# Kernel optimization log

Hardware: AMD Instinct MI355X
Metric: run time of the kernel (lower is better)

The kernel has to match this reference:

```python
import jax, jax.numpy as jnp
import numpy as np

N, E, D, F, L = 50000, 250000, 128, 12, 4
EPS_POS = 1e-6
EPS_LN = 1e-5


def setup_inputs() -> dict:
    key = jax.random.key(0)
    ks = iter(jax.random.split(key, 40))
    w = lambda *s: jax.random.normal(next(ks), s, dtype=jnp.float32) * 0.05
    inp = {
        'node_features': jax.random.normal(next(ks), (N, F), dtype=jnp.float32),
        'pos': jax.random.normal(next(ks), (N, 2), dtype=jnp.float32),
        'edge_attr_raw': jax.random.normal(next(ks), (E, F), dtype=jnp.float32),
        'node_proj_w': w(F, D), 'node_proj_b': jnp.zeros((D,), jnp.float32),
        'edge_proj_w': w(F, D), 'edge_proj_b': jnp.zeros((D,), jnp.float32),
        'edge_w1': w(L, 2 * D + 1, D), 'edge_b1': jnp.zeros((L, D), jnp.float32),
        'edge_w2': w(L, D, D), 'edge_b2': jnp.zeros((L, D), jnp.float32),
        'node_w1': w(L, 2 * D, D), 'node_b1': jnp.zeros((L, D), jnp.float32),
        'node_w2': w(L, D, D), 'node_b2': jnp.zeros((L, D), jnp.float32),
        'pos_w1': w(L, D + 1, 1), 'pos_b1': jnp.zeros((L, 1), jnp.float32),
        'pos_w2': w(L, 1, 1), 'pos_b2': jnp.zeros((L, 1), jnp.float32),
        'ln_g': jnp.ones((D,), jnp.float32), 'ln_b': jnp.zeros((D,), jnp.float32),
        'edge_index': jax.random.randint(next(ks), (2, E), 0, N, dtype=jnp.int32),
    }
    return inp


def reference(node_features, pos, edge_attr_raw,
              node_proj_w, node_proj_b, edge_proj_w, edge_proj_b,
              edge_w1, edge_b1, edge_w2, edge_b2,
              node_w1, node_b1, node_w2, node_b2,
              pos_w1, pos_b1, pos_w2, pos_b2,
              ln_g, ln_b, edge_index):
    src, tgt = edge_index[0], edge_index[1]
    n = node_features.shape[0]
    x = node_features @ node_proj_w + node_proj_b          # [N, D]
    # edge_projection output is concatenated then sliced away in the original
    # (edge_input[:, :2D+1]); it is mathematically dead but computed faithfully.
    _edge_attr = edge_attr_raw @ edge_proj_w + edge_proj_b  # dead
    p = pos                                                  # [N, 2]
    for l in range(L):
        xs, xt = x[src], x[tgt]                              # [E, D]
        ps, pt = p[src], p[tgt]                              # [E, 2]
        dist = jnp.linalg.norm(ps - pt, axis=1, keepdims=True)  # [E, 1]
        e_in = jnp.concatenate([xs, xt, dist], axis=1)       # [E, 2D+1]
        msg = jax.nn.silu(e_in @ edge_w1[l] + edge_b1[l]) @ edge_w2[l] + edge_b2[l]
        pos_diff = pt - ps
        pos_unit = pos_diff / (jnp.linalg.norm(pos_diff, axis=1, keepdims=True) + EPS_POS)
        pw = jax.nn.silu(jnp.concatenate([msg, dist], axis=1) @ pos_w1[l] + pos_b1[l])
        pw = pw @ pos_w2[l] + pos_b2[l]                       # [E, 1]
        p = p + jax.ops.segment_sum(pos_unit * pw, tgt, num_segments=n)
        agg = jax.ops.segment_sum(msg, tgt, num_segments=n)  # [N, D]
        n_in = jnp.concatenate([x, agg], axis=1)              # [N, 2D]
        x = x + (jax.nn.silu(n_in @ node_w1[l] + node_b1[l]) @ node_w2[l] + node_b2[l])
    mu = jnp.mean(x, axis=-1, keepdims=True)
    var = jnp.mean(jnp.square(x - mu), axis=-1, keepdims=True)
    x = (x - mu) * jax.lax.rsqrt(var + EPS_LN) * ln_g + ln_b
    return x[None]                                            # [1, N, D]
```

## Files before the change

kernel.cpp:

```cpp
#include <hip/hip_runtime.h>
#include <hip/hip_bf16.h>


#define NNODES 50000
#define NEDGES 250000
#define NTILES 3125
#define MMGRID 512
#define RGRID  1024

typedef unsigned short u16;
typedef __attribute__((ext_vector_type(8))) short bf16x8;
typedef __attribute__((ext_vector_type(4))) float floatx4;

__device__ __forceinline__ float b2f(u16 h){ unsigned u=((unsigned)h)<<16; float f; __builtin_memcpy(&f,&u,4); return f; }
__device__ __forceinline__ u16 f2b(float f){ unsigned u; __builtin_memcpy(&u,&f,4); u = u + 0x7FFFu + ((u>>16)&1u); return (u16)(u>>16); }
__device__ __forceinline__ float siluf(float x){ return x*__builtin_amdgcn_rcpf(1.f+__expf(-x)); }
__device__ __forceinline__ float ldf(const void* p, long i, int isbf){
  return isbf ? b2f(((const u16*)p)[i]) : ((const float*)p)[i];
}
__device__ __forceinline__ long swz(long row, int col){
  return (row>>4)*2048 + (long)(((col>>4)*4 + (int)(row&3))*64 + (((int)(row&15))>>2)*16 + (col&15));
}

__global__ void detect_kernel(const void* lng, int* flag){
  if (threadIdx.x==0 && blockIdx.x==0) *flag = (((const u16*)lng)[0] != 0) ? 1 : 0;
}

#define SU_W12   192
#define SU_EBW   704
#define SU_W2P   708
#define SU_PPARM 712
#define SU_PROJ  713
#define SU_CVTP  25713
#define SU_END   26104
__global__ __launch_bounds__(256) void setup_kernel(
    const void* __restrict__ ew1, const void* __restrict__ ew2,
    const void* __restrict__ nw1, const void* __restrict__ nw2,
    u16* __restrict__ packed,
    const void* __restrict__ eb2, const void* __restrict__ pw1,
    const void* __restrict__ pb1, const void* __restrict__ pw2v, const void* __restrict__ pb2,
    float* __restrict__ w2p, float* __restrict__ c2p, float* __restrict__ pparm,
    float* __restrict__ ebW,
    const void* __restrict__ nf, const void* __restrict__ npw, const void* __restrict__ npb,
    u16* __restrict__ xb,
    const void* __restrict__ pos, float* __restrict__ pf,
    const int* __restrict__ flagp)
{
  const int isbf = *flagp;
  const int b = blockIdx.x, tid = threadIdx.x;
  __shared__ float red[128];
  if (b < SU_W12){
    int t = b*256 + tid;
    int m = t >> 11; int r = t & 2047;
    int lane = r & 63; int ntk = r >> 6;
    int kk = ntk >> 3, nt = ntk & 7;
    int l = m/6, w = m%6;
    const void* src; long off;
    switch(w){
      case 0: src=ew1; off=(long)l*257*128;            break;
      case 1: src=ew1; off=(long)l*257*128 + 128*128;  break;
      case 2: src=ew2; off=(long)l*128*128;            break;
      case 3: src=nw1; off=(long)l*256*128;            break;
      case 4: src=nw1; off=(long)l*256*128 + 128*128;  break;
      default:src=nw2; off=(long)l*128*128;            break;
    }
    int c  = nt*16 + (lane & 15);
    int k0 = kk*32 + (lane >> 4)*8;
    u16 vals[8];
#pragma unroll
    for (int j=0;j<8;j++){
      long idx = off + (long)(k0+j)*128 + c;
      vals[j] = isbf ? ((const u16*)src)[idx] : f2b(((const float*)src)[idx]);
    }
    bf16x8 v; __builtin_memcpy(&v, vals, 16);
    *(bf16x8*)(packed + (long)t*8) = v;
  } else if (b < SU_EBW){
    int bb = b - SU_W12;
    int l = bb >> 7, k = bb & 127;
    if (tid < 128){
      int j = tid;
      long e2 = (long)l*16384 + (long)k*128;
      long nb = (long)l*256*128 + 128*128;
      float acc = 0.f;
      for (int d=0; d<128; d++)
        acc += ldf(ew2, e2 + d, isbf) * ldf(nw1, nb + (long)d*128 + j, isbf);
      int kk = k>>5, lane = ((k>>3)&3)*16 + (j&15), nt = j>>4, jj = k&7;
      packed[(long)(24+l)*16384 + (long)((kk*8+nt)*64 + lane)*8 + jj] = f2b(acc);
    }
  } else if (b < SU_W2P){
    int l = b - SU_EBW;
    if (tid < 128){
      int j = tid;
      long nb = (long)l*256*128 + 128*128;
      float acc = 0.f;
      for (int d=0; d<128; d++)
        acc += ldf(eb2, (long)l*128 + d, isbf) * ldf(nw1, nb + (long)d*128 + j, isbf);
      ebW[l*128+j] = acc;
    }
  } else if (b < SU_PPARM){
    int l = b - SU_W2P;
    int i = tid;
    long Woff = (long)l*128*128, poff = (long)l*129;
    if (i < 128){
      float acc = 0.f;
      for (int j=0;j<128;j++) acc += ldf(ew2, Woff + (long)i*128 + j, isbf) * ldf(pw1, poff + j, isbf);
      w2p[l*128+i] = acc;
      red[i] = ldf(eb2, (long)l*128 + i, isbf) * ldf(pw1, poff + i, isbf);
    }
    __syncthreads();
    for (int st=64; st>0; st>>=1){ if (i<st) red[i]+=red[i+st]; __syncthreads(); }
    if (i==0) c2p[l] = red[0];
  } else if (b == SU_PPARM){
    int l = tid;
    if (l < 4){
      pparm[l*4+0] = ldf(pw1, (long)l*129 + 128, isbf);
      pparm[l*4+1] = ldf(pb1, l, isbf);
      pparm[l*4+2] = ldf(pw2v, l, isbf);
      pparm[l*4+3] = ldf(pb2, l, isbf);
    }
  } else if (b < SU_CVTP){
    int n = (b - SU_PROJ)*2 + (tid>>7), d = tid & 127;
    if (n < NNODES){
      float acc = ldf(npb, d, isbf);
#pragma unroll
      for (int f=0; f<12; f++) acc += ldf(nf, (long)n*12+f, isbf) * ldf(npw, f*128+d, isbf);
      xb[swz(n, d)] = f2b(acc);
    }
  } else {
    int i = (b - SU_CVTP)*256 + tid;
    if (i < 2*NNODES) pf[i] = ldf(pos, i, isbf);
  }
}

__global__ __launch_bounds__(256) void hist_kernel(const int* __restrict__ tgt, int* __restrict__ cnt, int E){
  int i = blockIdx.x*256 + threadIdx.x;
  if (i < E) atomicAdd(&cnt[tgt[i]], 1);
}

__global__ __launch_bounds__(256) void bsum_kernel(const int* __restrict__ cnt, int* __restrict__ bsum, int N){
  int i = blockIdx.x*256 + threadIdx.x;
  int v = (i < N) ? cnt[i] : 0;
#pragma unroll
  for (int off=32; off; off>>=1) v += __shfl_down(v, off);
  __shared__ int ws[4];
  if ((threadIdx.x & 63) == 0) ws[threadIdx.x>>6] = v;
  __syncthreads();
  if (threadIdx.x == 0) bsum[blockIdx.x] = ws[0]+ws[1]+ws[2]+ws[3];
}

__global__ __launch_bounds__(256) void bscan_kernel(int* __restrict__ bsum, int nb){
  __shared__ int lds[256];
  int i = threadIdx.x;
  int v = (i < nb) ? bsum[i] : 0;
  lds[i] = v; __syncthreads();
#pragma unroll
  for (int off=1; off<256; off<<=1){
    int t = (i>=off)? lds[i-off] : 0; __syncthreads();
    lds[i] += t; __syncthreads();
  }
  if (i < nb) bsum[i] = lds[i] - v;
}

__global__ __launch_bounds__(256) void csr_kernel(
    const int* __restrict__ cnt, const int* __restrict__ bsum,
    int* __restrict__ rowptr, int* __restrict__ cursor, float* __restrict__ degf, int N)
{
  __shared__ int lds[256];
  int i = blockIdx.x*256 + threadIdx.x;
  int c = (i < N) ? cnt[i] : 0;
  lds[threadIdx.x] = c; __syncthreads();
#pragma unroll
  for (int off=1; off<256; off<<=1){
    int t = (threadIdx.x>=off)? lds[threadIdx.x-off] : 0; __syncthreads();
    lds[threadIdx.x] += t; __syncthreads();
  }
  int run = bsum[blockIdx.x] + lds[threadIdx.x] - c;
  if (i < N){
    rowptr[i] = run; cursor[i] = run; degf[i] = (float)c;
    if (i == N-1) rowptr[N] = run + c;
  }
}

__global__ __launch_bounds__(256) void scatter_kernel(
    const int* __restrict__ src, const int* __restrict__ tgt,
    int* __restrict__ cursor, int* __restrict__ permsrc, int E)
{
  int e = blockIdx.x*256 + threadIdx.x;
  if (e >= E) return;
  int t = tgt[e];
  int p = atomicAdd(&cursor[t], 1);
  permsrc[p] = src[e];
}

__global__ __launch_bounds__(256) void mm_ab_kernel(
    const u16* __restrict__ X, const u16* __restrict__ Wa, const u16* __restrict__ Wb,
    const void* __restrict__ bias, long bias_off,
    u16* __restrict__ Ab, u16* __restrict__ Bb, const int* __restrict__ flagp)
{
  extern __shared__ u16 wlds[];
  const int tid = threadIdx.x, wave = tid>>6, lane = tid&63;
  const int isbf = *flagp;
  const int lr = lane&15, lg = lane>>4;
  for (int i=tid; i<2048; i+=256){
    *(bf16x8*)(wlds + (long)i*8)          = *(const bf16x8*)(Wa + (long)i*8);
    *(bf16x8*)(wlds + 16384 + (long)i*8)  = *(const bf16x8*)(Wb + (long)i*8);
  }
  float biasv[8];
#pragma unroll
  for (int nt=0;nt<8;nt++) biasv[nt] = ldf(bias, bias_off + nt*16 + lr, isbf);
  int aoff[4];
#pragma unroll
  for (int kk=0;kk<4;kk++) aoff[kk] = ((2*kk + (lg>>1))*4 + (lr&3))*64 + (lr>>2)*16 + (lg&1)*8;
  u16* sw = wlds + 32768 + (wave<<11);
  __syncthreads();
  for (int tile = blockIdx.x*4 + wave; tile < NTILES; tile += MMGRID*4){
    const u16* xt = X + (long)tile*2048;
    bf16x8 a[4];
#pragma unroll
    for (int kk=0;kk<4;kk++) a[kk] = *(const bf16x8*)(xt + aoff[kk]);
    floatx4 accA[8], accB[8];
#pragma unroll
    for (int i=0;i<8;i++){ accA[i]=(floatx4){0,0,0,0}; accB[i]=(floatx4){0,0,0,0}; }
#pragma unroll
    for (int kk=0;kk<4;kk++){
#pragma unroll
      for (int nt=0;nt<8;nt++){
        bf16x8 ba = *(const bf16x8*)(wlds + ((kk*8+nt)*64 + lane)*8);
        accA[nt] = __builtin_amdgcn_mfma_f32_16x16x32_bf16(a[kk], ba, accA[nt], 0, 0, 0);
        bf16x8 bb = *(const bf16x8*)(wlds + 16384 + ((kk*8+nt)*64 + lane)*8);
        accB[nt] = __builtin_amdgcn_mfma_f32_16x16x32_bf16(a[kk], bb, accB[nt], 0, 0, 0);
      }
    }
    u16* at = Ab + (long)tile*2048;
#pragma unroll
    for (int r=0;r<4;r++){
#pragma unroll
      for (int nt=0;nt<8;nt++) sw[(lg*4+r)*128 + nt*16 + lr] = f2b(accA[nt][r] + biasv[nt]);
    }
#pragma unroll
    for (int j=0;j<4;j++){
      bf16x8 v = *(const bf16x8*)(sw + j*512 + lane*8);
      *(bf16x8*)(at + j*512 + lane*8) = v;
    }
    u16* bt = Bb + (long)tile*2048;
#pragma unroll
    for (int r=0;r<4;r++){
#pragma unroll
      for (int nt=0;nt<8;nt++) sw[(lg*4+r)*128 + nt*16 + lr] = f2b(accB[nt][r]);
    }
#pragma unroll
    for (int j=0;j<4;j++){
      bf16x8 v = *(const bf16x8*)(sw + j*512 + lane*8);
      *(bf16x8*)(bt + j*512 + lane*8) = v;
    }
  }
}

__global__ __launch_bounds__(256) void mm_hidden_kernel(
    const u16* __restrict__ X, const u16* __restrict__ H,
    const u16* __restrict__ W1, const u16* __restrict__ W2,
    const void* __restrict__ nb1, long nb1_off,
    const float* __restrict__ degf, const float* __restrict__ ebW,
    u16* __restrict__ hb, const int* __restrict__ flagp)
{
  extern __shared__ u16 wlds[];
  const int tid = threadIdx.x, wave = tid>>6, lane = tid&63;
  const int isbf = *flagp;
  const int lr = lane&15, lg = lane>>4;
  for (int i=tid; i<2048; i+=256){
    *(bf16x8*)(wlds + (long)i*8)          = *(const bf16x8*)(W1 + (long)i*8);
    *(bf16x8*)(wlds + 16384 + (long)i*8)  = *(const bf16x8*)(W2 + (long)i*8);
  }
  float nb1v[8], ebv[8];
#pragma unroll
  for (int nt=0;nt<8;nt++){ int col=nt*16+lr; nb1v[nt]=ldf(nb1, nb1_off+col, isbf); ebv[nt]=ebW[col]; }
  int aoff[4];
#pragma unroll
  for (int kk=0;kk<4;kk++) aoff[kk] = ((2*kk + (lg>>1))*4 + (lr&3))*64 + (lr>>2)*16 + (lg&1)*8;
  __syncthreads();
  for (int tile = blockIdx.x*4 + wave; tile < NTILES; tile += MMGRID*4){
    const u16* xt = X + (long)tile*2048;
    const u16* hr = H + ((long)tile*16 + lr)*128;
    bf16x8 ax[4], ah[4];
#pragma unroll
    for (int kk=0;kk<4;kk++){
      ax[kk] = *(const bf16x8*)(xt + aoff[kk]);
      ah[kk] = *(const bf16x8*)(hr + kk*32 + lg*8);
    }
    floatx4 acc[8];
#pragma unroll
    for (int i=0;i<8;i++) acc[i]=(floatx4){0,0,0,0};
#pragma unroll
    for (int kk=0;kk<4;kk++){
#pragma unroll
      for (int nt=0;nt<8;nt++){
        bf16x8 b1 = *(const bf16x8*)(wlds + ((kk*8+nt)*64 + lane)*8);
        acc[nt] = __builtin_amdgcn_mfma_f32_16x16x32_bf16(ax[kk], b1, acc[nt], 0, 0, 0);
        bf16x8 b2 = *(const bf16x8*)(wlds + 16384 + ((kk*8+nt)*64 + lane)*8);
        acc[nt] = __builtin_amdgcn_mfma_f32_16x16x32_bf16(ah[kk], b2, acc[nt], 0, 0, 0);
      }
    }
    float dv[4];
#pragma unroll
    for (int r=0;r<4;r++) dv[r] = degf[(long)tile*16 + lg*4 + r];
    u16* ot = hb + (long)tile*2048;
#pragma unroll
    for (int r=0;r<4;r++){
#pragma unroll
      for (int nt=0;nt<8;nt++){
        ot[(nt*4+r)*64 + lane] = f2b(siluf(acc[nt][r] + nb1v[nt] + dv[r]*ebv[nt]));
      }
    }
  }
}

template<int LN>
__global__ __launch_bounds__(256) void mm_res_kernel(
    const u16* __restrict__ H, const u16* __restrict__ W,
    const void* __restrict__ nb2, long nb2_off,
    u16* __restrict__ xb,
    const void* __restrict__ lng, const void* __restrict__ lnb, void* __restrict__ outp,
    const int* __restrict__ flagp)
{
  extern __shared__ u16 wlds[];
  const int tid = threadIdx.x, wave = tid>>6, lane = tid&63;
  const int isbf = *flagp;
  const int lr = lane&15, lg = lane>>4;
  for (int i=tid; i<2048; i+=256)
    *(bf16x8*)(wlds + (long)i*8) = *(const bf16x8*)(W + (long)i*8);
  float nb2v[8];
#pragma unroll
  for (int nt=0;nt<8;nt++) nb2v[nt] = ldf(nb2, nb2_off + nt*16 + lr, isbf);
  float gv[8], bvv[8];
  if (LN){
#pragma unroll
    for (int nt=0;nt<8;nt++){ int col=nt*16+lr; gv[nt]=ldf(lng,col,isbf); bvv[nt]=ldf(lnb,col,isbf); }
  }
  int aoff[4];
#pragma unroll
  for (int kk=0;kk<4;kk++) aoff[kk] = ((2*kk + (lg>>1))*4 + (lr&3))*64 + (lr>>2)*16 + (lg&1)*8;
  __syncthreads();
  for (int tile = blockIdx.x*4 + wave; tile < NTILES; tile += RGRID*4){
    const u16* ht = H + (long)tile*2048;
    bf16x8 a[4];
#pragma unroll
    for (int kk=0;kk<4;kk++) a[kk] = *(const bf16x8*)(ht + aoff[kk]);
    floatx4 acc[8];
#pragma unroll
    for (int i=0;i<8;i++) acc[i]=(floatx4){0,0,0,0};
#pragma unroll
    for (int kk=0;kk<4;kk++){
#pragma unroll
      for (int nt=0;nt<8;nt++){
        bf16x8 b = *(const bf16x8*)(wlds + ((kk*8+nt)*64 + lane)*8);
        acc[nt] = __builtin_amdgcn_mfma_f32_16x16x32_bf16(a[kk], b, acc[nt], 0, 0, 0);
      }
    }
    u16* xt = xb + (long)tile*2048;
#pragma unroll
    for (int r=0;r<4;r++){
#pragma unroll
      for (int nt=0;nt<8;nt++){
        int o = (nt*4+r)*64 + lane;
        float v = acc[nt][r] + nb2v[nt] + b2f(xt[o]);
        acc[nt][r] = v;
        if (!LN) xt[o] = f2b(v);
      }
    }
    if (LN){
      float s[4] = {0,0,0,0}, q[4] = {0,0,0,0};
#pragma unroll
      for (int r=0;r<4;r++){
#pragma unroll
        for (int nt=0;nt<8;nt++){ float v = acc[nt][r]; s[r] += v; q[r] += v*v; }
      }
#pragma unroll
      for (int mask=1; mask<16; mask<<=1){
#pragma unroll
        for (int r=0;r<4;r++){ s[r] += __shfl_xor(s[r], mask); q[r] += __shfl_xor(q[r], mask); }
      }
#pragma unroll
      for (int r=0;r<4;r++){
        long row = (long)tile*16 + lg*4 + r;
        float mu = s[r]*(1.f/128.f);
        float var = q[r]*(1.f/128.f) - mu*mu;
        float inv = rsqrtf(var + 1e-5f);
#pragma unroll
        for (int nt=0;nt<8;nt++){
          int col = nt*16 + lr;
          float y = (acc[nt][r]-mu)*inv*gv[nt] + bvv[nt];
          if (isbf) ((u16*)outp)[row*128+col] = f2b(y);
          else      ((float*)outp)[row*128+col] = y;
        }
      }
    }
  }
}

__global__ __launch_bounds__(256) void agg_kernel(
    const int* __restrict__ rowptr, const int* __restrict__ permsrc,
    const float* __restrict__ pf_in,
    const u16* __restrict__ A, const u16* __restrict__ B,
    const void* __restrict__ ew1, long w1c_off,
    const float* __restrict__ w2p, const float* __restrict__ c2pl,
    const float* __restrict__ pp,
    u16* __restrict__ Hb, float* __restrict__ pf_out, int N,
    const int* __restrict__ flagp)
{
  const int isbf = *flagp;
  int tid = threadIdx.x, lane = tid & 63;
  int t = blockIdx.x*4 + (tid>>6);
  if (t >= N) return;
  int tu = __builtin_amdgcn_readfirstlane(t);
  float c0 = ldf(ew1, w1c_off + 2*lane,     isbf);
  float c1 = ldf(ew1, w1c_off + 2*lane + 1, isbf);
  float2 wp = *(const float2*)(w2p + 2*lane);
  float c2 = c2pl[0];
  float p0 = pp[0], p1 = pp[1], p2 = pp[2], p3 = pp[3];
  int jb = rowptr[tu], je = rowptr[tu+1];
  float2 pt = *(const float2*)(pf_in + 2*(long)tu);
  unsigned bv = *(const unsigned*)(B + (long)tu*128 + 2*lane);
  float b0 = b2f((u16)bv), b1 = b2f((u16)(bv>>16));
  float h0a = 0.f, h1a = 0.f, dpx = 0.f, dpy = 0.f;
  for (int j0 = jb; j0 < je; j0 += 4){
    int m = je - j0; if (m > 4) m = 4;
    int s[4]; float2 ps[4]; unsigned av[4];
    float part[4], dist[4], dxv[4], dyv[4];
#pragma unroll
    for (int c=0;c<4;c++) if (c<m) s[c] = permsrc[j0+c];
#pragma unroll
    for (int c=0;c<4;c++) if (c<m){
      ps[c] = *(const float2*)(pf_in + 2*(long)s[c]);
      av[c] = *(const unsigned*)(A + (long)s[c]*128 + 2*lane);
    }
#pragma unroll
    for (int c=0;c<4;c++){
      if (c<m){
        float dx = pt.x - ps[c].x, dy = pt.y - ps[c].y;
        float d2 = dx*dx + dy*dy;
        float dd = __builtin_amdgcn_sqrtf(d2);
        float h0 = siluf(b2f((u16)av[c])       + b0 + dd*c0);
        float h1 = siluf(b2f((u16)(av[c]>>16)) + b1 + dd*c1);
        h0a += h0; h1a += h1;
        part[c] = h0*wp.x + h1*wp.y;
        dist[c] = dd; dxv[c] = dx; dyv[c] = dy;
      } else part[c] = 0.f;
    }
#pragma unroll
    for (int off=32; off; off>>=1){
#pragma unroll
      for (int c=0;c<4;c++) part[c] += __shfl_xor(part[c], off);
    }
#pragma unroll
    for (int c=0;c<4;c++){
      if (c<m){
        float spre = part[c] + c2 + dist[c]*p0 + p1;
        float pwv  = siluf(spre)*p2 + p3;
        float inv  = __builtin_amdgcn_rcpf(dist[c] + 1e-6f);
        dpx += dxv[c]*inv*pwv; dpy += dyv[c]*inv*pwv;
      }
    }
  }
  *(unsigned*)(Hb + (long)tu*128 + 2*lane) = (unsigned)f2b(h0a) | ((unsigned)f2b(h1a)<<16);
  if (lane == 0){
    float2 o; o.x = pt.x + dpx; o.y = pt.y + dpy;
    *(float2*)(pf_out + 2*(long)tu) = o;
  }
}

extern "C" void kernel_launch(void* const* d_in, const int* in_sizes, int n_in,
                              void* d_out, int out_size, void* d_ws, size_t ws_size,
                              hipStream_t stream)
{
  const void* nf  = d_in[0];
  const void* pos = d_in[1];
  const void* npw = d_in[3];
  const void* npb = d_in[4];
  const void* ew1 = d_in[7];
  const void* eb1 = d_in[8];
  const void* ew2 = d_in[9];
  const void* eb2 = d_in[10];
  const void* nw1 = d_in[11];
  const void* nb1 = d_in[12];
  const void* nw2 = d_in[13];
  const void* nb2 = d_in[14];
  const void* pw1 = d_in[15];
  const void* pb1 = d_in[16];
  const void* pw2 = d_in[17];
  const void* pb2 = d_in[18];
  const void* lng = d_in[19];
  const void* lnb = d_in[20];
  const int* eidx = (const int*)d_in[21];
  const int N = NNODES, E = NEDGES;
  const int* srcp = eidx;
  const int* tgtp = eidx + E;

  char* w = (char*)d_ws;
  size_t off = 0;
  auto alloc = [&](size_t bytes)->char* { char* p = w + off; off += (bytes + 255)/256*256; return p; };
  u16*   xb    = (u16*)  alloc((size_t)N*128*2);
  u16*   Ab    = (u16*)  alloc((size_t)N*128*2);
  u16*   Bb    = (u16*)  alloc((size_t)N*128*2);
  u16*   Hb    = (u16*)  alloc((size_t)N*128*2);
  float* pf0   = (float*)alloc((size_t)N*2*4);
  float* pf1   = (float*)alloc((size_t)N*2*4);
  int*   cnt   = (int*)  alloc((size_t)N*4);
  int*   rowptr= (int*)  alloc((size_t)(N+1)*4);
  int*   cursor= (int*)  alloc((size_t)N*4);
  float* degf  = (float*)alloc((size_t)N*4);
  int*   perm  = (int*)  alloc((size_t)E*4);
  int*   bsum  = (int*)  alloc(256*4);
  u16*   pk    = (u16*)  alloc((size_t)28*16384*2);
  float* ebW   = (float*)alloc(4*128*4);
  float* w2p   = (float*)alloc(4*128*4);
  float* c2p   = (float*)alloc(4*4);
  float* pparm = (float*)alloc(16*4);
  int*   flag  = (int*)  alloc(4);
  u16* hb = Ab;

  const int NB = (N + 255)/256;
  detect_kernel<<<1, 64, 0, stream>>>(lng, flag);
  hipMemsetAsync(cnt, 0, (size_t)N*4, stream);
  hist_kernel<<<(E+255)/256, 256, 0, stream>>>(tgtp, cnt, E);
  bsum_kernel<<<NB, 256, 0, stream>>>(cnt, bsum, N);
  bscan_kernel<<<1, 256, 0, stream>>>(bsum, NB);
  csr_kernel<<<NB, 256, 0, stream>>>(cnt, bsum, rowptr, cursor, degf, N);
  scatter_kernel<<<(E+255)/256, 256, 0, stream>>>(srcp, tgtp, cursor, perm, E);
  setup_kernel<<<SU_END, 256, 0, stream>>>(
      ew1, ew2, nw1, nw2, pk,
      eb2, pw1, pb1, pw2, pb2,
      w2p, c2p, pparm, ebW,
      nf, npw, npb, xb,
      pos, pf0, flag);

  mm_ab_kernel<<<MMGRID, 256, 81920, stream>>>(xb, pk + 0*16384, pk + 1*16384,
                                               eb1, 0, Ab, Bb, flag);
  for (int l = 0; l < 4; l++){
    const u16* NW1a = pk + (l*6+3)*16384;
    const u16* NW2p = pk + (l*6+5)*16384;
    const u16* W12p = pk + (24+l)*16384;
    float* pin  = (l & 1) ? pf1 : pf0;
    float* pout = (l & 1) ? pf0 : pf1;

    agg_kernel<<<(N+3)/4, 256, 0, stream>>>(
        rowptr, perm, pin, Ab, Bb,
        ew1, (long)l*257*128 + 256*128,
        w2p + l*128, c2p + l, pparm + l*4,
        Hb, pout, N, flag);
    mm_hidden_kernel<<<MMGRID, 256, 65536, stream>>>(
        xb, Hb, NW1a, W12p, nb1, (long)l*128, degf, ebW + l*128, hb, flag);
    if (l < 3){
      mm_res_kernel<0><<<RGRID, 256, 32768, stream>>>(
          hb, NW2p, nb2, (long)l*128, xb, nullptr, nullptr, nullptr, flag);
      mm_ab_kernel<<<MMGRID, 256, 81920, stream>>>(
          xb, pk + ((l+1)*6+0)*16384, pk + ((l+1)*6+1)*16384,
          eb1, (long)(l+1)*128, Ab, Bb, flag);
    } else {
      mm_res_kernel<1><<<RGRID, 256, 32768, stream>>>(
          hb, NW2p, nb2, (long)l*128, xb, lng, lnb, d_out, flag);
    }
  }
}
```

Before: 518.0 us.

## Read MFMA weight fragments directly from global memory instead of LDS staging

The node-side matmul kernels stop copying the full weight matrices into shared memory and instead load each B fragment straight from global (cached) memory. Only a small per-wave staging buffer stays in LDS, and launch bounds request higher occupancy, with the grid raised to 782 blocks so every tile gets a wave. The final LayerNorm output in bf16 mode is now written as coalesced 16-byte stores through LDS. The tradeoff is repeated global/L2 weight reads per tile in place of LDS reads, in return for removing the per-block LDS fill and barrier and allowing more resident blocks.

Measured after the change: 1.182 ms. 128% more time.

```diff
diff --git a/kernel.cpp b/kernel.cpp
--- a/kernel.cpp
+++ b/kernel.cpp
@@ -5,7 +5,7 @@
 #define NNODES 50000
 #define NEDGES 250000
 #define NTILES 3125
-#define MMGRID 512
+#define MMGRID 782
 #define RGRID  1024
 
 typedef unsigned short u16;
@@ -192,27 +192,22 @@
   permsrc[p] = src[e];
 }
 
-__global__ __launch_bounds__(256) void mm_ab_kernel(
+__global__ __launch_bounds__(256, 3) void mm_ab_kernel(
     const u16* __restrict__ X, const u16* __restrict__ Wa, const u16* __restrict__ Wb,
     const void* __restrict__ bias, long bias_off,
     u16* __restrict__ Ab, u16* __restrict__ Bb, const int* __restrict__ flagp)
 {
-  extern __shared__ u16 wlds[];
+  __shared__ u16 sw_[8192];
   const int tid = threadIdx.x, wave = tid>>6, lane = tid&63;
   const int isbf = *flagp;
   const int lr = lane&15, lg = lane>>4;
-  for (int i=tid; i<2048; i+=256){
-    *(bf16x8*)(wlds + (long)i*8)          = *(const bf16x8*)(Wa + (long)i*8);
-    *(bf16x8*)(wlds + 16384 + (long)i*8)  = *(const bf16x8*)(Wb + (long)i*8);
-  }
   float biasv[8];
 #pragma unroll
   for (int nt=0;nt<8;nt++) biasv[nt] = ldf(bias, bias_off + nt*16 + lr, isbf);
   int aoff[4];
 #pragma unroll
   for (int kk=0;kk<4;kk++) aoff[kk] = ((2*kk + (lg>>1))*4 + (lr&3))*64 + (lr>>2)*16 + (lg&1)*8;
-  u16* sw = wlds + 32768 + (wave<<11);
-  __syncthreads();
+  u16* sw = sw_ + (wave<<11);
   for (int tile = blockIdx.x*4 + wave; tile < NTILES; tile += MMGRID*4){
     const u16* xt = X + (long)tile*2048;
     bf16x8 a[4];
@@ -225,9 +220,9 @@
     for (int kk=0;kk<4;kk++){
 #pragma unroll
       for (int nt=0;nt<8;nt++){
-        bf16x8 ba = *(const bf16x8*)(wlds + ((kk*8+nt)*64 + lane)*8);
+        bf16x8 ba = *(const bf16x8*)(Wa + ((kk*8+nt)*64 + lane)*8);
         accA[nt] = __builtin_amdgcn_mfma_f32_16x16x32_bf16(a[kk], ba, accA[nt], 0, 0, 0);
-        bf16x8 bb = *(const bf16x8*)(wlds + 16384 + ((kk*8+nt)*64 + lane)*8);
+        bf16x8 bb = *(const bf16x8*)(Wb + ((kk*8+nt)*64 + lane)*8);
         accB[nt] = __builtin_amdgcn_mfma_f32_16x16x32_bf16(a[kk], bb, accB[nt], 0, 0, 0);
       }
     }
@@ -256,28 +251,22 @@
   }
 }
 
-__global__ __launch_bounds__(256) void mm_hidden_kernel(
+__global__ __launch_bounds__(256, 4) void mm_hidden_kernel(
     const u16* __restrict__ X, const u16* __restrict__ H,
     const u16* __restrict__ W1, const u16* __restrict__ W2,
     const void* __restrict__ nb1, long nb1_off,
     const float* __restrict__ degf, const float* __restrict__ ebW,
     u16* __restrict__ hb, const int* __restrict__ flagp)
 {
-  extern __shared__ u16 wlds[];
   const int tid = threadIdx.x, wave = tid>>6, lane = tid&63;
   const int isbf = *flagp;
   const int lr = lane&15, lg = lane>>4;
-  for (int i=tid; i<2048; i+=256){
-    *(bf16x8*)(wlds + (long)i*8)          = *(const bf16x8*)(W1 + (long)i*8);
-    *(bf16x8*)(wlds + 16384 + (long)i*8)  = *(const bf16x8*)(W2 + (long)i*8);
-  }
   float nb1v[8], ebv[8];
 #pragma unroll
   for (int nt=0;nt<8;nt++){ int col=nt*16+lr; nb1v[nt]=ldf(nb1, nb1_off+col, isbf); ebv[nt]=ebW[col]; }
   int aoff[4];
 #pragma unroll
   for (int kk=0;kk<4;kk++) aoff[kk] = ((2*kk + (lg>>1))*4 + (lr&3))*64 + (lr>>2)*16 + (lg&1)*8;
-  __syncthreads();
   for (int tile = blockIdx.x*4 + wave; tile < NTILES; tile += MMGRID*4){
     const u16* xt = X + (long)tile*2048;
     const u16* hr = H + ((long)tile*16 + lr)*128;
@@ -294,9 +283,9 @@
     for (int kk=0;kk<4;kk++){
 #pragma unroll
       for (int nt=0;nt<8;nt++){
-        bf16x8 b1 = *(const bf16x8*)(wlds + ((kk*8+nt)*64 + lane)*8);
+        bf16x8 b1 = *(const bf16x8*)(W1 + ((kk*8+nt)*64 + lane)*8);
         acc[nt] = __builtin_amdgcn_mfma_f32_16x16x32_bf16(ax[kk], b1, acc[nt], 0, 0, 0);
-        bf16x8 b2 = *(const bf16x8*)(wlds + 16384 + ((kk*8+nt)*64 + lane)*8);
+        bf16x8 b2 = *(const bf16x8*)(W2 + ((kk*8+nt)*64 + lane)*8);
         acc[nt] = __builtin_amdgcn_mfma_f32_16x16x32_bf16(ah[kk], b2, acc[nt], 0, 0, 0);
       }
     }
@@ -315,19 +304,17 @@
 }
 
 template<int LN>
-__global__ __launch_bounds__(256) void mm_res_kernel(
+__global__ __launch_bounds__(256, 4) void mm_res_kernel(
     const u16* __restrict__ H, const u16* __restrict__ W,
     const void* __restrict__ nb2, long nb2_off,
     u16* __restrict__ xb,
     const void* __restrict__ lng, const void* __restrict__ lnb, void* __restrict__ outp,
     const int* __restrict__ flagp)
 {
-  extern __shared__ u16 wlds[];
+  __shared__ u16 sw_[8192];
   const int tid = threadIdx.x, wave = tid>>6, lane = tid&63;
   const int isbf = *flagp;
   const int lr = lane&15, lg = lane>>4;
-  for (int i=tid; i<2048; i+=256)
-    *(bf16x8*)(wlds + (long)i*8) = *(const bf16x8*)(W + (long)i*8);
   float nb2v[8];
 #pragma unroll
   for (int nt=0;nt<8;nt++) nb2v[nt] = ldf(nb2, nb2_off + nt*16 + lr, isbf);
@@ -339,7 +326,7 @@
   int aoff[4];
 #pragma unroll
   for (int kk=0;kk<4;kk++) aoff[kk] = ((2*kk + (lg>>1))*4 + (lr&3))*64 + (lr>>2)*16 + (lg&1)*8;
-  __syncthreads();
+  u16* sw = sw_ + (wave<<11);
   for (int tile = blockIdx.x*4 + wave; tile < NTILES; tile += RGRID*4){
     const u16* ht = H + (long)tile*2048;
     bf16x8 a[4];
@@ -352,7 +339,7 @@
     for (int kk=0;kk<4;kk++){
 #pragma unroll
       for (int nt=0;nt<8;nt++){
-        bf16x8 b = *(const bf16x8*)(wlds + ((kk*8+nt)*64 + lane)*8);
+        bf16x8 b = *(const bf16x8*)(W + ((kk*8+nt)*64 + lane)*8);
         acc[nt] = __builtin_amdgcn_mfma_f32_16x16x32_bf16(a[kk], b, acc[nt], 0, 0, 0);
       }
     }
@@ -379,18 +366,35 @@
 #pragma unroll
         for (int r=0;r<4;r++){ s[r] += __shfl_xor(s[r], mask); q[r] += __shfl_xor(q[r], mask); }
       }
+      float mu4[4], inv4[4];
 #pragma unroll
       for (int r=0;r<4;r++){
-        long row = (long)tile*16 + lg*4 + r;
         float mu = s[r]*(1.f/128.f);
         float var = q[r]*(1.f/128.f) - mu*mu;
-        float inv = rsqrtf(var + 1e-5f);
-#pragma unroll
-        for (int nt=0;nt<8;nt++){
-          int col = nt*16 + lr;
-          float y = (acc[nt][r]-mu)*inv*gv[nt] + bvv[nt];
-          if (isbf) ((u16*)outp)[row*128+col] = f2b(y);
-          else      ((float*)outp)[row*128+col] = y;
+        mu4[r] = mu; inv4[r] = rsqrtf(var + 1e-5f);
+      }
+      if (isbf){
+#pragma unroll
+        for (int r=0;r<4;r++){
+#pragma unroll
+          for (int nt=0;nt<8;nt++)
+            sw[(lg*4+r)*128 + nt*16 + lr] = f2b((acc[nt][r]-mu4[r])*inv4[r]*gv[nt] + bvv[nt]);
+        }
+        u16* ot = (u16*)outp + (long)tile*2048;
+#pragma unroll
+        for (int j=0;j<4;j++){
+          bf16x8 v = *(const bf16x8*)(sw + j*512 + lane*8);
+          *(bf16x8*)(ot + j*512 + lane*8) = v;
+        }
+      } else {
+#pragma unroll
+        for (int r=0;r<4;r++){
+          long row = (long)tile*16 + lg*4 + r;
+#pragma unroll
+          for (int nt=0;nt<8;nt++){
+            int col = nt*16 + lr;
+            ((float*)outp)[row*128+col] = (acc[nt][r]-mu4[r])*inv4[r]*gv[nt] + bvv[nt];
+          }
         }
       }
     }
@@ -533,8 +537,8 @@
       nf, npw, npb, xb,
       pos, pf0, flag);
 
-  mm_ab_kernel<<<MMGRID, 256, 81920, stream>>>(xb, pk + 0*16384, pk + 1*16384,
-                                               eb1, 0, Ab, Bb, flag);
+  mm_ab_kernel<<<MMGRID, 256, 0, stream>>>(xb, pk + 0*16384, pk + 1*16384,
+                                           eb1, 0, Ab, Bb, flag);
   for (int l = 0; l < 4; l++){
     const u16* NW1a = pk + (l*6+3)*16384;
     const u16* NW2p = pk + (l*6+5)*16384;
@@ -547,16 +551,16 @@
         ew1, (long)l*257*128 + 256*128,
         w2p + l*128, c2p + l, pparm + l*4,
         Hb, pout, N, flag);
-    mm_hidden_kernel<<<MMGRID, 256, 65536, stream>>>(
+    mm_hidden_kernel<<<MMGRID, 256, 0, stream>>>(
         xb, Hb, NW1a, W12p, nb1, (long)l*128, degf, ebW + l*128, hb, flag);
     if (l < 3){
-      mm_res_kernel<0><<<RGRID, 256, 32768, stream>>>(
+      mm_res_kernel<0><<<RGRID, 256, 0, stream>>>(
           hb, NW2p, nb2, (long)l*128, xb, nullptr, nullptr, nullptr, flag);
-      mm_ab_kernel<<<MMGRID, 256, 81920, stream>>>(
+      mm_ab_kernel<<<MMGRID, 256, 0, stream>>>(
           xb, pk + ((l+1)*6+0)*16384, pk + ((l+1)*6+1)*16384,
           eb1, (long)(l+1)*128, Ab, Bb, flag);
     } else {
-      mm_res_kernel<1><<<RGRID, 256, 32768, stream>>>(
+      mm_res_kernel<1><<<RGRID, 256, 0, stream>>>(
           hb, NW2p, nb2, (long)l*128, xb, lng, lnb, d_out, flag);
     }
   }
```
